# Optimization experiments

Measured on AMD Instinct MI355X. Metric: run time of the kernel, lower is better.

## Reference

```python
import jax, jax.numpy as jnp
import numpy as np

P, D, NF, NR, ND, EF, ER = 512, 128, 50000, 50000, 100000, 400000, 400000
BASELINE = 6.0


def setup_inputs() -> dict:
    key = jax.random.key(0)
    ctr = [0]
    def nk():
        ctr[0] += 1
        return jax.random.fold_in(key, ctr[0])
    def nrm(shape, scale=1.0):
        return jax.random.normal(nk(), shape, dtype=jnp.float32) * scale
    def uni(shape):
        return jax.random.uniform(nk(), shape, dtype=jnp.float32)
    def lin(fi, fo):
        return nrm((fi, fo), fi ** -0.5), jnp.zeros((fo,), jnp.float32)
    inp = {}
    inp['target_features'] = nrm((P,))
    inp['form_features'] = nrm((NF, P))
    inp['role_features'] = nrm((NR, P))
    inp['form_binds_y'] = BASELINE + nrm((EF,))
    inp['form_binds_w'] = uni((EF,))
    inp['role_binds_y'] = BASELINE + nrm((ER,))
    inp['role_binds_w'] = uni((ER,))
    inp['form_diff_w'] = uni((NF,)) + 0.01
    inp['role_diff_w'] = uni((NR,)) + 0.01
    inp['trust_vector'] = uni((3,))
    inp['drug_features'] = nrm((ND, D))
    inp['form_w1'], inp['form_b1'] = lin(P, P); inp['form_a1'] = jnp.full((1,), 0.25, jnp.float32)
    inp['form_w2'], inp['form_b2'] = lin(P, P)
    inp['role_w1'], inp['role_b1'] = lin(P, P); inp['role_a1'] = jnp.full((1,), 0.25, jnp.float32)
    inp['role_w2'], inp['role_b2'] = lin(P, P)
    inp['q_w'], inp['q_b'] = lin(P, D)
    inp['k_w'], inp['k_b'] = lin(D, D)
    inp['v_w'], inp['v_b'] = lin(D, D)
    inp['layer_emb'] = nrm((2, 16))
    inp['attn_w1'], inp['attn_b1'] = lin(2 * P + 16, 128)
    inp['attn_w2'], inp['attn_b2'] = lin(128, 64)
    inp['attn_w3'], inp['attn_b3'] = lin(64, 1)
    inp['mix_w1'], inp['mix_b1'] = lin(2 * D + 3, 64); inp['mix_a'] = jnp.full((1,), 0.25, jnp.float32)
    inp['mix_w2'], inp['mix_b2'] = lin(64, 2)
    inp['int_w1'], inp['int_b1'] = lin(D, P); inp['int_a'] = jnp.full((1,), 0.25, jnp.float32)
    inp['int_w2'], inp['int_b2'] = lin(P, P)
    inp['norm_w'] = jnp.ones((P,), jnp.float32)
    inp['norm_b'] = jnp.zeros((P,), jnp.float32)
    inp['delta_gate'] = jnp.float32(0.5)
    inp['form_neighbors'] = jnp.arange(NF, dtype=jnp.int32)
    inp['role_neighbors'] = jnp.arange(NR, dtype=jnp.int32)
    inp['form_binds_src'] = jax.random.randint(nk(), (EF,), 0, NF, dtype=jnp.int32)
    inp['form_binds_dst'] = jax.random.randint(nk(), (EF,), 0, ND, dtype=jnp.int32)
    inp['role_binds_src'] = jax.random.randint(nk(), (ER,), 0, NR, dtype=jnp.int32)
    inp['role_binds_dst'] = jax.random.randint(nk(), (ER,), 0, ND, dtype=jnp.int32)
    return inp


def _prelu(x, a):
    return jnp.where(x >= 0, x, a * x)


def _mlp2(x, w1, b1, a, w2, b2):
    return _prelu(x @ w1 + b1, a) @ w2 + b2


def _ln(x, w=None, b=None, eps=1e-5):
    m = jnp.mean(x, -1, keepdims=True)
    v = jnp.mean((x - m) ** 2, -1, keepdims=True)
    y = (x - m) * jax.lax.rsqrt(v + eps)
    return y if w is None else y * w + b


def _pref(z, nid, src, dst, y, w, drugs, q_w, q_b, k_w, k_b, v_w, v_b):
    # segment-softmax attention over (neighbor protein -> drug) bipartite edges
    N = nid.shape[0]
    order = jnp.argsort(nid)
    s = nid[order]
    pos = jnp.searchsorted(s, src)
    clip = jnp.minimum(pos, N - 1)
    valid = (pos < N) & (s[clip] == src)
    seg = jnp.where(valid, order[clip], N)  # invalid edges -> dump segment N
    q = z @ q_w + q_b                       # [D]
    d = drugs[dst]                          # [E, D] gather
    k = d @ k_w + k_b
    v = (d @ v_w + v_b) * ((y - BASELINE) * w)[:, None]
    logits = (k @ q) / (k.shape[-1] ** 0.5)
    mx = jax.ops.segment_max(logits, seg, num_segments=N + 1)
    mx = jnp.where(jnp.isfinite(mx), mx, 0.0)
    ex = jnp.where(valid, jnp.exp(logits - mx[seg]), 0.0)
    den = jax.ops.segment_sum(ex, seg, num_segments=N + 1) + 1e-12
    attn = ex / den[seg]
    return jax.ops.segment_sum(v * attn[:, None], seg, num_segments=N + 1)[:N]


def _attn_logits(z, zn, lemb, w1, b1, w2, b2, w3, b3):
    N = zn.shape[0]
    x = jnp.concatenate([jnp.broadcast_to(z, (N, z.shape[0])), zn,
                         jnp.broadcast_to(lemb, (N, lemb.shape[0]))], axis=-1)
    h = jax.nn.leaky_relu(x @ w1 + b1, 0.2)
    h = jax.nn.leaky_relu(h @ w2 + b2, 0.2)
    return (h @ w3 + b3)[:, 0]


def _core(fl, form_neighbors, role_neighbors, form_binds_src, form_binds_dst, role_binds_src, role_binds_dst):
    (target_features, form_features, role_features, form_binds_y, form_binds_w,
     role_binds_y, role_binds_w, form_diff_w, role_diff_w, trust_vector, drug_features,
     form_w1, form_b1, form_a1, form_w2, form_b2,
     role_w1, role_b1, role_a1, role_w2, role_b2,
     q_w, q_b, k_w, k_b, v_w, v_b, layer_emb,
     attn_w1, attn_b1, attn_w2, attn_b2, attn_w3, attn_b3,
     mix_w1, mix_b1, mix_a, mix_w2, mix_b2,
     int_w1, int_b1, int_a, int_w2, int_b2,
     norm_w, norm_b, delta_gate) = fl
    z_form = _mlp2(target_features, form_w1, form_b1, form_a1, form_w2, form_b2)
    z_role = _mlp2(target_features, role_w1, role_b1, role_a1, role_w2, role_b2)
    z = 0.5 * (z_form + z_role)
    form_feats = _mlp2(form_features, form_w1, form_b1, form_a1, form_w2, form_b2)
    role_feats = _mlp2(role_features, role_w1, role_b1, role_a1, role_w2, role_b2)
    form_msgs = _pref(z, form_neighbors, form_binds_src, form_binds_dst, form_binds_y, form_binds_w, drug_features, q_w, q_b, k_w, k_b, v_w, v_b)
    role_msgs = _pref(z, role_neighbors, role_binds_src, role_binds_dst, role_binds_y, role_binds_w, drug_features, q_w, q_b, k_w, k_b, v_w, v_b)
    form_logits = _attn_logits(z, form_feats, layer_emb[0], attn_w1, attn_b1, attn_w2, attn_b2, attn_w3, attn_b3)
    role_logits = _attn_logits(z, role_feats, layer_emb[1], attn_w1, attn_b1, attn_w2, attn_b2, attn_w3, attn_b3)
    form_attn = jax.nn.softmax(form_logits + jnp.log(jnp.maximum(form_diff_w, 1e-12)))
    role_attn = jax.nn.softmax(role_logits + jnp.log(jnp.maximum(role_diff_w, 1e-12)))
    v_form = form_attn @ form_msgs
    v_role = role_attn @ role_msgs
    mixer_in = jnp.concatenate([v_form, v_role, trust_vector])
    lw = jax.nn.softmax(_mlp2(mixer_in, mix_w1, mix_b1, mix_a, mix_w2, mix_b2))
    w_form, w_role = lw[0], lw[1]
    v_prior = w_form * v_form + w_role * v_role
    form_delta = form_attn @ (z[None, :] - form_feats)
    role_delta = role_attn @ (z[None, :] - role_feats)
    delta_raw = w_form * form_delta + w_role * role_delta
    delta_mean = delta_gate * _ln(delta_raw)
    z_refined = _ln(z + _mlp2(v_prior, int_w1, int_b1, int_a, int_w2, int_b2), norm_w, norm_b)
    return z_refined, v_prior, delta_mean


def reference(target_features, form_features, role_features, form_binds_y, form_binds_w, role_binds_y, role_binds_w, form_diff_w, role_diff_w, trust_vector, drug_features, form_w1, form_b1, form_a1, form_w2, form_b2, role_w1, role_b1, role_a1, role_w2, role_b2, q_w, q_b, k_w, k_b, v_w, v_b, layer_emb, attn_w1, attn_b1, attn_w2, attn_b2, attn_w3, attn_b3, mix_w1, mix_b1, mix_a, mix_w2, mix_b2, int_w1, int_b1, int_a, int_w2, int_b2, norm_w, norm_b, delta_gate, form_neighbors, role_neighbors, form_binds_src, form_binds_dst, role_binds_src, role_binds_dst):
    fl = (target_features, form_features, role_features, form_binds_y, form_binds_w,
          role_binds_y, role_binds_w, form_diff_w, role_diff_w, trust_vector, drug_features,
          form_w1, form_b1, form_a1, form_w2, form_b2,
          role_w1, role_b1, role_a1, role_w2, role_b2,
          q_w, q_b, k_w, k_b, v_w, v_b, layer_emb,
          attn_w1, attn_b1, attn_w2, attn_b2, attn_w3, attn_b3,
          mix_w1, mix_b1, mix_a, mix_w2, mix_b2,
          int_w1, int_b1, int_a, int_w2, int_b2,
          norm_w, norm_b, delta_gate)
    return _core(fl, form_neighbors, role_neighbors, form_binds_src, form_binds_dst, role_binds_src, role_binds_dst)
```

## Files before the change

kernel.cpp:

```cpp
#include <hip/hip_runtime.h>

#define NFN 50000
#define NDR 100000
#define NE  400000
#define MT  391
#define M0PAD 50048

__device__ __forceinline__ float bf2f(unsigned short u) {
    return __uint_as_float(((unsigned)u) << 16);
}
__device__ __forceinline__ unsigned short f2bf(float f) {
    unsigned u = __float_as_uint(f);
    unsigned r = 0x7FFFu + ((u >> 16) & 1u);
    return (unsigned short)((u + r) >> 16);
}

typedef __attribute__((ext_vector_type(8))) short bf16x8;
typedef __attribute__((ext_vector_type(4))) float f32x4;

struct KArgs {
    const float *tf, *ff, *rf, *fby, *fbw, *rby, *rbw, *fdw, *rdw, *trust, *drugs;
    const float *fw1, *fb1, *fa1, *fw2, *fb2, *rw1, *rb1, *ra1, *rw2, *rb2;
    const float *qw, *qb, *kw, *kb, *vw, *vb, *lemb;
    const float *aw1, *ab1, *aw2, *ab2, *aw3, *ab3;
    const float *mw1, *mb1, *ma, *mw2, *mb2;
    const float *iw1, *ib1, *ia, *iw2, *ib2;
    const float *nw, *nb, *dgate;
    const int *fsrc, *fdst, *rsrc, *rdst;
    float *shf, *shr;
    float *svf, *svr;
    float *gdenf, *gdenr;
    float *edenf, *edenr;
    float *cdf, *cdr;
    float *hraw;
    float *zraw;
    float *qraw;
    float *b1f, *b1r;
    float *sfr;
    float *o2raw;
    float *qk, *c0, *pe;
    unsigned short *w1tf, *w1tr;
    unsigned short *w2atf, *w2atr;
    unsigned short *aw2t;
    float *nexf, *nexr;
    unsigned short *H;
    unsigned short *Xb;
    float *hi;
    float *wfwr;
    float *out;
};

__global__ __launch_bounds__(512) void kA(KArgs A) {
    const int b = blockIdx.x;
    const int side = b >> 5, chunk = b & 31;
    const int tt = threadIdx.x;
    const float* w1 = side ? A.rw1 : A.fw1;
    float acc = 0.f;
    const int i0 = chunk * 16;
#pragma unroll
    for (int k = 0; k < 16; k++) {
        int i = i0 + k;
        acc = fmaf(A.tf[i], w1[(size_t)i * 512 + tt], acc);
    }
    atomicAdd(&A.hraw[side * 512 + tt], acc);
}

__global__ __launch_bounds__(512) void kB(KArgs A) {
    const int b = blockIdx.x;
    const int side = b >> 4, chunk = b & 15;
    const int tt = threadIdx.x;
    const float* w2 = side ? A.rw2 : A.fw2;
    const float* b1 = side ? A.rb1 : A.fb1;
    const float aa = (side ? A.ra1 : A.fa1)[0];
    float acc = 0.f;
    const int i0 = chunk * 32;
    for (int k = 0; k < 32; k++) {
        int i = i0 + k;
        float h = A.hraw[side * 512 + i] + b1[i];
        h = h >= 0.f ? h : aa * h;
        acc = fmaf(h, w2[(size_t)i * 512 + tt], acc);
    }
    if (b == 0) acc += A.fb2[tt] + A.rb2[tt];
    atomicAdd(&A.zraw[tt], acc);
}

__global__ __launch_bounds__(512) void kC1(KArgs A) {
    const int b = blockIdx.x;
    const int t = threadIdx.x;
    const int j = t & 127, isub = t >> 7;
    if (b < 8) {
        const int i0 = b * 64 + isub * 16;
        float acc = 0.f;
        for (int k = 0; k < 16; k++) {
            int i = i0 + k;
            acc = fmaf(0.5f * A.zraw[i], A.qw[(size_t)i * 128 + j], acc);
        }
        atomicAdd(&A.qraw[j], acc);
        if (b == 0 && t < 128) atomicAdd(&A.qraw[t], A.qb[t]);
    } else if (b < 16) {
        const int chunk = b - 8;
        const int i0 = chunk * 64 + isub * 16;
        float acc = 0.f;
        for (int k = 0; k < 16; k++) {
            int i = i0 + k;
            acc = fmaf(0.5f * A.zraw[i], A.aw1[(size_t)i * 128 + j], acc);
            acc = fmaf(A.fb2[i], A.aw1[(size_t)(512 + i) * 128 + j], acc);
        }
        atomicAdd(&A.b1f[j], acc);
        if (b == 8 && t < 128) {
            float c = A.ab1[t];
            for (int l = 0; l < 16; l++) c = fmaf(A.lemb[l], A.aw1[(size_t)(1024 + l) * 128 + t], c);
            atomicAdd(&A.b1f[t], c);
        }
    } else {
        const int chunk = b - 16;
        const int i0 = chunk * 64 + isub * 16;
        float acc = 0.f;
        for (int k = 0; k < 16; k++) {
            int i = i0 + k;
            acc = fmaf(0.5f * A.zraw[i], A.aw1[(size_t)i * 128 + j], acc);
            acc = fmaf(A.rb2[i], A.aw1[(size_t)(512 + i) * 128 + j], acc);
        }
        atomicAdd(&A.b1r[j], acc);
        if (b == 16 && t < 128) {
            float c = A.ab1[t];
            for (int l = 0; l < 16; l++) c = fmaf(A.lemb[16 + l], A.aw1[(size_t)(1024 + l) * 128 + t], c);
            atomicAdd(&A.b1r[t], c);
        }
    }
}

__global__ __launch_bounds__(256) void kC2(KArgs A) {
    const int t = threadIdx.x;
    __shared__ float sq[128];
    if (t < 128) sq[t] = A.qraw[t];
    __syncthreads();
    if (t < 128) {
        float s = 0.f;
        for (int j = 0; j < 128; j++) s = fmaf(A.kw[t * 128 + j], sq[j], s);
        A.qk[t] = s;
    } else if (t == 128) {
        float c = 0.f;
        for (int j = 0; j < 128; j++) c = fmaf(A.kb[j], sq[j], c);
        A.c0[0] = c;
    }
}

__global__ __launch_bounds__(256) void k_cvtX2(KArgs A) {
    const int XN4 = NFN * 512 / 4;
    const int P4 = M0PAD * 512 / 4;
    int idx = blockIdx.x * 256 + threadIdx.x;
    const int stride = gridDim.x * 256;
    for (; idx < 2 * XN4; idx += stride) {
        const int side = idx >= XN4;
        const int li = idx - side * XN4;
        float4 v = ((const float4*)(side ? A.rf : A.ff))[li];
        uint2 o;
        o.x = (unsigned)f2bf(v.x) | ((unsigned)f2bf(v.y) << 16);
        o.y = (unsigned)f2bf(v.z) | ((unsigned)f2bf(v.w) << 16);
        ((uint2*)A.Xb)[(size_t)side * P4 + li] = o;
    }
}

__global__ __launch_bounds__(512) void k_cvtW(KArgs A) {
    const int side = blockIdx.x >> 9;
    const int k = blockIdx.x & 511;
    const int n = threadIdx.x;
    const float* w1 = side ? A.rw1 : A.fw1;
    unsigned short* o = side ? A.w1tr : A.w1tf;
    o[(size_t)n * 512 + k] = f2bf(w1[k * 512 + n]);
}

__global__ __launch_bounds__(128) void k_cvtA2(KArgs A) {
    const int j = blockIdx.x;
    const int i = threadIdx.x;
    A.aw2t[j * 128 + i] = f2bf(A.aw2[i * 64 + j]);
}

__global__ __launch_bounds__(128) void k_w2a(KArgs A) {
    const int side = blockIdx.x >> 9;
    const int i = blockIdx.x & 511;
    const int j = threadIdx.x;
    const float* w2 = side ? A.rw2 : A.fw2;
    unsigned short* outp = side ? A.w2atr : A.w2atf;
    float s = 0.f;
    for (int k = 0; k < 512; k++)
        s = fmaf(w2[i * 512 + k], A.aw1[(size_t)(512 + k) * 128 + j], s);
    outp[(size_t)j * 512 + i] = f2bf(s);
}

__global__ __launch_bounds__(256, 2)
void mfma_gemm(KArgs A) {
    __shared__ __align__(16) unsigned short Abuf[2][128 * 32];
    __shared__ __align__(16) unsigned short Bbuf[2][128 * 32];
    const int t = threadIdx.x;
    const int lane = t & 63, wv = t >> 6;
    const int p = blockIdx.x;
    const int L = (p & 7) * MT + (p >> 3);
    const int side = L >= (MT * 4);
    const int lbid = L - side * (MT * 4);
    const int m0l = (lbid >> 2) * 128, n0 = (lbid & 3) * 128;
    const unsigned short* __restrict__ Ab = A.Xb + (size_t)side * M0PAD * 512;
    const unsigned short* __restrict__ Bt = side ? A.w1tr : A.w1tf;
    const float* __restrict__ bias = side ? A.rb1 : A.fb1;
    const float aval = (side ? A.ra1 : A.fa1)[0];
    unsigned short* __restrict__ Cv = A.H + (size_t)side * M0PAD * 512;
    const int wm = (wv >> 1) * 64, wn = (wv & 1) * 64;
    const int lm = lane & 15, ko = lane >> 4;
    const int K = 512;

    f32x4 acc[4][4];
#pragma unroll
    for (int i = 0; i < 4; i++)
#pragma unroll
        for (int j = 0; j < 4; j++) acc[i][j] = (f32x4){0.f, 0.f, 0.f, 0.f};

    auto stage = [&](int buf, int k0) {
#pragma unroll
        for (int ii = 0; ii < 2; ii++) {
            const int inst = wv * 2 + ii;
            const int rl = inst * 16 + (lane >> 2);
            const int sl = (lane & 3) ^ ((rl >> 1) & 3);
            int ar = m0l + rl; if (ar >= NFN) ar = NFN - 1;
            __builtin_amdgcn_global_load_lds(
                (const __attribute__((address_space(1))) void*)(Ab + (size_t)ar * K + k0 + sl * 8),
                (__attribute__((address_space(3))) void*)(&Abuf[buf][inst * 512]), 16, 0, 0);
            __builtin_amdgcn_global_load_lds(
                (const __attribute__((address_space(1))) void*)(Bt + (size_t)(n0 + rl) * K + k0 + sl * 8),
                (__attribute__((address_space(3))) void*)(&Bbuf[buf][inst * 512]), 16, 0, 0);
        }
    };

    auto compute = [&](int buf) {
        bf16x8 af[4], bfr[4];
#pragma unroll
        for (int mi = 0; mi < 4; mi++) {
            int row = wm + mi * 16 + lm;
            af[mi] = *(const bf16x8*)&Abuf[buf][row * 32 + ((ko ^ ((row >> 1) & 3)) * 8)];
        }
#pragma unroll
        for (int ni = 0; ni < 4; ni++) {
            int col = wn + ni * 16 + lm;
            bfr[ni] = *(const bf16x8*)&Bbuf[buf][col * 32 + ((ko ^ ((col >> 1) & 3)) * 8)];
        }
#pragma unroll
        for (int mi = 0; mi < 4; mi++)
#pragma unroll
            for (int ni = 0; ni < 4; ni++)
                acc[mi][ni] = __builtin_amdgcn_mfma_f32_16x16x32_bf16(af[mi], bfr[ni], acc[mi][ni], 0, 0, 0);
    };

    stage(0, 0);
    __syncthreads();
    for (int kt = 0; kt < 16; kt++) {
        if (kt + 1 < 16) stage((kt + 1) & 1, (kt + 1) * 32);
        compute(kt & 1);
        __syncthreads();
    }

#pragma unroll
    for (int mi = 0; mi < 4; mi++) {
#pragma unroll
        for (int reg = 0; reg < 4; reg++) {
            int row = m0l + wm + mi * 16 + ko * 4 + reg;
#pragma unroll
            for (int ni = 0; ni < 4; ni++) {
                int col = n0 + wn + ni * 16 + lm;
                float v = acc[mi][ni][reg] + bias[col];
                v = v >= 0.f ? v : aval * v;
                Cv[(size_t)row * 512 + col] = f2bf(v);
            }
        }
    }
}

__global__ __launch_bounds__(256, 2)
void gemm_logits(KArgs A) {
    __shared__ __align__(16) unsigned short Abuf[2][128 * 32];
    __shared__ __align__(16) unsigned short Bbuf[2][128 * 32];
    __shared__ __align__(16) unsigned short Gs[128][136];
    __shared__ float ps[128];
    __shared__ float red2[128];
    __shared__ float snex[128];
    const int bid = blockIdx.x;
    const int side = bid >= MT;
    const int m0l = (bid - side * MT) * 128;
    const unsigned short* __restrict__ Ab = A.H + (size_t)side * M0PAD * 512;
    const unsigned short* __restrict__ Bt = side ? A.w2atr : A.w2atf;
    const float* __restrict__ bias = side ? A.b1r : A.b1f;
    const float* __restrict__ dw = side ? A.rdw : A.fdw;
    float* __restrict__ nex = side ? A.nexr : A.nexf;
    float* __restrict__ gden = side ? A.gdenr : A.gdenf;
    const int t = threadIdx.x;
    const int lane = t & 63, wv = t >> 6;
    const int wm = (wv >> 1) * 64, wn = (wv & 1) * 64;
    const int lm = lane & 15, ko = lane >> 4;
    const int K = 512;

    f32x4 acc[4][4];
#pragma unroll
    for (int i = 0; i < 4; i++)
#pragma unroll
        for (int j = 0; j < 4; j++) acc[i][j] = (f32x4){0.f, 0.f, 0.f, 0.f};

    auto stage = [&](int buf, int k0) {
#pragma unroll
        for (int ii = 0; ii < 2; ii++) {
            const int inst = wv * 2 + ii;
            const int rl = inst * 16 + (lane >> 2);
            const int sl = (lane & 3) ^ ((rl >> 1) & 3);
            int ar = m0l + rl; if (ar >= NFN) ar = NFN - 1;
            __builtin_amdgcn_global_load_lds(
                (const __attribute__((address_space(1))) void*)(Ab + (size_t)ar * K + k0 + sl * 8),
                (__attribute__((address_space(3))) void*)(&Abuf[buf][inst * 512]), 16, 0, 0);
            __builtin_amdgcn_global_load_lds(
                (const __attribute__((address_space(1))) void*)(Bt + (size_t)rl * K + k0 + sl * 8),
                (__attribute__((address_space(3))) void*)(&Bbuf[buf][inst * 512]), 16, 0, 0);
        }
    };

    auto compute = [&](int buf) {
        bf16x8 af[4], bfr[4];
#pragma unroll
        for (int mi = 0; mi < 4; mi++) {
            int row = wm + mi * 16 + lm;
            af[mi] = *(const bf16x8*)&Abuf[buf][row * 32 + ((ko ^ ((row >> 1) & 3)) * 8)];
        }
#pragma unroll
        for (int ni = 0; ni < 4; ni++) {
            int col = wn + ni * 16 + lm;
            bfr[ni] = *(const bf16x8*)&Bbuf[buf][col * 32 + ((ko ^ ((col >> 1) & 3)) * 8)];
        }
#pragma unroll
        for (int mi = 0; mi < 4; mi++)
#pragma unroll
            for (int ni = 0; ni < 4; ni++)
                acc[mi][ni] = __builtin_amdgcn_mfma_f32_16x16x32_bf16(af[mi], bfr[ni], acc[mi][ni], 0, 0, 0);
    };

    stage(0, 0);
    __syncthreads();
    for (int kt = 0; kt < 16; kt++) {
        if (kt + 1 < 16) stage((kt + 1) & 1, (kt + 1) * 32);
        compute(kt & 1);
        __syncthreads();
    }

#pragma unroll
    for (int mi = 0; mi < 4; mi++) {
#pragma unroll
        for (int reg = 0; reg < 4; reg++) {
            int row_l = wm + mi * 16 + ko * 4 + reg;
#pragma unroll
            for (int ni = 0; ni < 4; ni++) {
                int col = wn + ni * 16 + lm;
                float v = acc[mi][ni][reg] + bias[col];
                v = v >= 0.f ? v : 0.2f * v;
                Gs[row_l][col] = f2bf(v);
            }
        }
    }
    __syncthreads();

    const int wr0 = wv * 32;
    float ab2v[4], aw3v[4];
#pragma unroll
    for (int ni = 0; ni < 4; ni++) {
        int col = ni * 16 + lm;
        ab2v[ni] = A.ab2[col];
        aw3v[ni] = A.aw3[col];
    }
    f32x4 acc2[2][4];
#pragma unroll
    for (int i = 0; i < 2; i++)
#pragma unroll
        for (int j = 0; j < 4; j++) acc2[i][j] = (f32x4){0.f, 0.f, 0.f, 0.f};
#pragma unroll
    for (int kk = 0; kk < 4; kk++) {
        bf16x8 ga[2], bb[4];
#pragma unroll
        for (int mi = 0; mi < 2; mi++)
            ga[mi] = *(const bf16x8*)&Gs[wr0 + mi * 16 + lm][kk * 32 + ko * 8];
#pragma unroll
        for (int ni = 0; ni < 4; ni++)
            bb[ni] = *(const bf16x8*)(A.aw2t + (size_t)(ni * 16 + lm) * 128 + kk * 32 + ko * 8);
#pragma unroll
        for (int mi = 0; mi < 2; mi++)
#pragma unroll
            for (int ni = 0; ni < 4; ni++)
                acc2[mi][ni] = __builtin_amdgcn_mfma_f32_16x16x32_bf16(ga[mi], bb[ni], acc2[mi][ni], 0, 0, 0);
    }
#pragma unroll
    for (int mi = 0; mi < 2; mi++) {
#pragma unroll
        for (int reg = 0; reg < 4; reg++) {
            float s = 0.f;
#pragma unroll
            for (int ni = 0; ni < 4; ni++) {
                float v = acc2[mi][ni][reg] + ab2v[ni];
                v = v >= 0.f ? v : 0.2f * v;
                s = fmaf(v, aw3v[ni], s);
            }
            s += __shfl_xor(s, 1, 64);
            s += __shfl_xor(s, 2, 64);
            s += __shfl_xor(s, 4, 64);
            s += __shfl_xor(s, 8, 64);
            if (lm == 0) ps[wr0 + mi * 16 + ko * 4 + reg] = s;
        }
    }
    __syncthreads();
    float val = 0.f;
    if (t < 128) {
        int node = m0l + t;
        if (node < NFN) {
            val = expf(ps[t] + A.ab3[0] + logf(fmaxf(dw[node], 1e-12f)));
            nex[node] = val;
        }
        snex[t] = val;
        red2[t] = val;
    }
    __syncthreads();
    if (t < 64) red2[t] += red2[t + 64];
    __syncthreads();
    if (t < 32) red2[t] += red2[t + 32];
    __syncthreads();
    if (t < 16) red2[t] += red2[t + 16];
    __syncthreads();
    if (t == 0) {
        float s = 0.f;
        for (int i = 0; i < 16; i++) s += red2[i];
        atomicAdd(gden, s);
    }
    {
        const unsigned short* Hrow = Ab + (size_t)m0l * 512;
        float a0 = 0.f, a1 = 0.f;
        for (int r = 0; r < 128; r += 2) {
            const float w0 = snex[r], w1 = snex[r + 1];
            const unsigned v0 = *(const unsigned*)(Hrow + (size_t)r * 512 + 2 * t);
            const unsigned v1 = *(const unsigned*)(Hrow + (size_t)(r + 1) * 512 + 2 * t);
            a0 = fmaf(w0, bf2f((unsigned short)(v0 & 0xFFFFu)), a0);
            a1 = fmaf(w0, bf2f((unsigned short)(v0 >> 16)), a1);
            a0 = fmaf(w1, bf2f((unsigned short)(v1 & 0xFFFFu)), a0);
            a1 = fmaf(w1, bf2f((unsigned short)(v1 >> 16)), a1);
        }
        float* SH = side ? A.shr : A.shf;
        atomicAdd(&SH[2 * t], a0);
        atomicAdd(&SH[2 * t + 1], a1);
    }
}

__global__ __launch_bounds__(256) void k_pd(KArgs A) {
    const int lane = threadIdx.x & 63;
    const int gw = blockIdx.x * 4 + (threadIdx.x >> 6);
    const int nw = gridDim.x * 4;
    const float2 qk2 = *(const float2*)(A.qk + 2 * lane);
    const float c0 = A.c0[0];
    for (int dr = gw; dr < NDR; dr += nw) {
        float2 dv = *(const float2*)(A.drugs + (size_t)dr * 128 + 2 * lane);
        float p = fmaf(dv.x, qk2.x, dv.y * qk2.y);
        for (int off = 32; off >= 1; off >>= 1) p += __shfl_xor(p, off, 64);
        if (lane == 0) A.pe[dr] = expf((p + c0) * 0.088388347648318447f);
    }
}

__global__ __launch_bounds__(256) void k_edge1(KArgs A) {
    const int side = blockIdx.y;
    const int* src = side ? A.rsrc : A.fsrc;
    const int* dst = side ? A.rdst : A.fdst;
    float* eden = side ? A.edenr : A.edenf;
    const int base = blockIdx.x * 1024 + threadIdx.x;
#pragma unroll
    for (int u = 0; u < 4; u++) {
        const int e = base + u * 256;
        if (e < NE) atomicAdd(&eden[src[e]], A.pe[dst[e]]);
    }
}

__global__ __launch_bounds__(256) void k_nfac(KArgs A) {
    const int side = blockIdx.y;
    const int n = blockIdx.x * 256 + threadIdx.x;
    if (n >= NFN) return;
    const float* nex = side ? A.nexr : A.nexf;
    float* eden = side ? A.edenr : A.edenf;
    const float invden = 1.0f / *(side ? A.gdenr : A.gdenf);
    eden[n] = nex[n] * invden / (eden[n] + 1e-12f);
}

__global__ __launch_bounds__(256) void k_edge2(KArgs A) {
    const int side = blockIdx.y;
    const int* src = side ? A.rsrc : A.fsrc;
    const int* dst = side ? A.rdst : A.fdst;
    const float* yy = side ? A.rby : A.fby;
    const float* ww = side ? A.rbw : A.fbw;
    const float* fac = side ? A.edenr : A.edenf;
    float* cd = side ? A.cdr : A.cdf;
    float* sv = side ? A.svr : A.svf;
    const int base = blockIdx.x * 1024 + threadIdx.x;
    float csum = 0.f;
#pragma unroll
    for (int u = 0; u < 4; u++) {
        const int e = base + u * 256;
        if (e < NE) {
            float coef = fac[src[e]] * A.pe[dst[e]] * ((yy[e] - 6.0f) * ww[e]);
            atomicAdd(&cd[dst[e]], coef);
            csum += coef;
        }
    }
    __shared__ float red[256];
    red[threadIdx.x] = csum; __syncthreads();
    for (int s2 = 128; s2 >= 1; s2 >>= 1) {
        if (threadIdx.x < s2) red[threadIdx.x] += red[threadIdx.x + s2];
        __syncthreads();
    }
    if (threadIdx.x == 0) atomicAdd(&sv[128], red[0]);
}

__global__ __launch_bounds__(256) void k_wsumD(KArgs A) {
    const int t = threadIdx.x;
    const int col = t & 127, rg = t >> 7;
    __shared__ float red[2][2][128];
    float af = 0.f, ar = 0.f;
    for (int dr = blockIdx.x * 2 + rg; dr < NDR; dr += gridDim.x * 2) {
        float cf = A.cdf[dr], cr = A.cdr[dr];
        float dv = A.drugs[(size_t)dr * 128 + col];
        af = fmaf(cf, dv, af);
        ar = fmaf(cr, dv, ar);
    }
    red[rg][0][col] = af; red[rg][1][col] = ar;
    __syncthreads();
    if (rg == 0) {
        atomicAdd(&A.svf[col], red[0][0][col] + red[1][0][col]);
        atomicAdd(&A.svr[col], red[0][1][col] + red[1][1][col]);
    }
}

__global__ __launch_bounds__(512) void kF1(KArgs A) {
    const int b = blockIdx.x;
    const int side = b >> 3, chunk = b & 7;
    const int tt = threadIdx.x;
    const float* w2 = side ? A.rw2 : A.fw2;
    const float* SH = side ? A.shr : A.shf;
    const float invden = 1.0f / *(side ? A.gdenr : A.gdenf);
    float acc = 0.f;
    const int i0 = chunk * 64;
    for (int k = 0; k < 64; k++) {
        int i = i0 + k;
        acc = fmaf(SH[i], w2[(size_t)i * 512 + tt], acc);
    }
    acc *= invden;
    if (chunk == 0) acc += (side ? A.rb2 : A.fb2)[tt];
    atomicAdd(&A.sfr[side * 512 + tt], acc);
}

__global__ __launch_bounds__(512) void kF2(KArgs A) {
    const int t = threadIdx.x;
    __shared__ float vform[128], vrole[128], vprior[128], mh[64], sw[2];
    if (t < 128) {
        float vf = A.svf[128] * A.vb[t];
        float vr = A.svr[128] * A.vb[t];
        for (int i = 0; i < 128; i++) {
            vf = fmaf(A.svf[i], A.vw[i * 128 + t], vf);
            vr = fmaf(A.svr[i], A.vw[i * 128 + t], vr);
        }
        vform[t] = vf; vrole[t] = vr;
    }
    __syncthreads();
    if (t < 64) {
        float m = A.mb1[t];
        for (int i = 0; i < 128; i++) m = fmaf(vform[i], A.mw1[i * 64 + t], m);
        for (int i = 0; i < 128; i++) m = fmaf(vrole[i], A.mw1[(128 + i) * 64 + t], m);
        for (int i = 0; i < 3; i++)   m = fmaf(A.trust[i], A.mw1[(256 + i) * 64 + t], m);
        float ma = A.ma[0];
        mh[t] = m >= 0.f ? m : ma * m;
    }
    __syncthreads();
    if (t < 2) {
        float o = A.mb2[t];
        for (int i = 0; i < 64; i++) o = fmaf(mh[i], A.mw2[i * 2 + t], o);
        sw[t] = o;
    }
    __syncthreads();
    const float mo = fmaxf(sw[0], sw[1]);
    const float e0 = expf(sw[0] - mo), e1 = expf(sw[1] - mo);
    const float wf = e0 / (e0 + e1), wr = e1 / (e0 + e1);
    if (t == 0) { A.wfwr[0] = wf; A.wfwr[1] = wr; }
    if (t < 128) {
        float vp = wf * vform[t] + wr * vrole[t];
        vprior[t] = vp;
        A.out[512 + t] = vp;
    }
    __syncthreads();
    float hi = A.ib1[t];
    for (int i = 0; i < 128; i++) hi = fmaf(vprior[i], A.iw1[(size_t)i * 512 + t], hi);
    float ia = A.ia[0];
    A.hi[t] = hi >= 0.f ? hi : ia * hi;
}

__global__ __launch_bounds__(512) void kF3(KArgs A) {
    const int chunk = blockIdx.x;
    const int tt = threadIdx.x;
    float acc = 0.f;
    const int i0 = chunk * 64;
    for (int k = 0; k < 64; k++) {
        int i = i0 + k;
        acc = fmaf(A.hi[i], A.iw2[(size_t)i * 512 + tt], acc);
    }
    if (chunk == 0) acc += A.ib2[tt];
    atomicAdd(&A.o2raw[tt], acc);
}

__global__ __launch_bounds__(512) void kF4(KArgs A) {
    const int t = threadIdx.x;
    __shared__ float red[512];
    const float wf = A.wfwr[0], wr = A.wfwr[1];
    const float zv = 0.5f * A.zraw[t];
    float dr_ = zv - wf * A.sfr[t] - wr * A.sfr[512 + t];
    red[t] = dr_; __syncthreads();
    for (int s = 256; s >= 1; s >>= 1) { if (t < s) red[t] += red[t + s]; __syncthreads(); }
    float mean = red[0] * (1.f / 512.f); __syncthreads();
    float dd = dr_ - mean;
    red[t] = dd * dd; __syncthreads();
    for (int s = 256; s >= 1; s >>= 1) { if (t < s) red[t] += red[t + s]; __syncthreads(); }
    float var = red[0] * (1.f / 512.f); __syncthreads();
    A.out[640 + t] = A.dgate[0] * (dd * rsqrtf(var + 1e-5f));
    float zin = zv + A.o2raw[t];
    red[t] = zin; __syncthreads();
    for (int s = 256; s >= 1; s >>= 1) { if (t < s) red[t] += red[t + s]; __syncthreads(); }
    float mean2 = red[0] * (1.f / 512.f); __syncthreads();
    float d2 = zin - mean2;
    red[t] = d2 * d2; __syncthreads();
    for (int s = 256; s >= 1; s >>= 1) { if (t < s) red[t] += red[t + s]; __syncthreads(); }
    float var2 = red[0] * (1.f / 512.f);
    A.out[t] = (d2 * rsqrtf(var2 + 1e-5f)) * A.nw[t] + A.nb[t];
}

extern "C" void kernel_launch(void* const* d_in, const int* in_sizes, int n_in,
                              void* d_out, int out_size, void* d_ws, size_t ws_size,
                              hipStream_t stream) {
    (void)in_sizes; (void)n_in; (void)out_size;
    KArgs A;
    A.tf    = (const float*)d_in[0];
    A.ff    = (const float*)d_in[1];
    A.rf    = (const float*)d_in[2];
    A.fby   = (const float*)d_in[3];
    A.fbw   = (const float*)d_in[4];
    A.rby   = (const float*)d_in[5];
    A.rbw   = (const float*)d_in[6];
    A.fdw   = (const float*)d_in[7];
    A.rdw   = (const float*)d_in[8];
    A.trust = (const float*)d_in[9];
    A.drugs = (const float*)d_in[10];
    A.fw1 = (const float*)d_in[11]; A.fb1 = (const float*)d_in[12]; A.fa1 = (const float*)d_in[13];
    A.fw2 = (const float*)d_in[14]; A.fb2 = (const float*)d_in[15];
    A.rw1 = (const float*)d_in[16]; A.rb1 = (const float*)d_in[17]; A.ra1 = (const float*)d_in[18];
    A.rw2 = (const float*)d_in[19]; A.rb2 = (const float*)d_in[20];
    A.qw = (const float*)d_in[21]; A.qb = (const float*)d_in[22];
    A.kw = (const float*)d_in[23]; A.kb = (const float*)d_in[24];
    A.vw = (const float*)d_in[25]; A.vb = (const float*)d_in[26];
    A.lemb = (const float*)d_in[27];
    A.aw1 = (const float*)d_in[28]; A.ab1 = (const float*)d_in[29];
    A.aw2 = (const float*)d_in[30]; A.ab2 = (const float*)d_in[31];
    A.aw3 = (const float*)d_in[32]; A.ab3 = (const float*)d_in[33];
    A.mw1 = (const float*)d_in[34]; A.mb1 = (const float*)d_in[35]; A.ma = (const float*)d_in[36];
    A.mw2 = (const float*)d_in[37]; A.mb2 = (const float*)d_in[38];
    A.iw1 = (const float*)d_in[39]; A.ib1 = (const float*)d_in[40]; A.ia = (const float*)d_in[41];
    A.iw2 = (const float*)d_in[42]; A.ib2 = (const float*)d_in[43];
    A.nw = (const float*)d_in[44]; A.nb = (const float*)d_in[45];
    A.dgate = (const float*)d_in[46];
    A.fsrc = (const int*)d_in[49];
    A.fdst = (const int*)d_in[50];
    A.rsrc = (const int*)d_in[51];
    A.rdst = (const int*)d_in[52];
    A.out = (float*)d_out;

    char* w = (char*)d_ws;
    size_t off = 0;
    auto alloc = [&](size_t bytes) -> void* {
        void* p = w + off;
        off = (off + bytes + 255) & ~(size_t)255;
        return p;
    };
    A.shf   = (float*)alloc(512 * 4);
    A.shr   = (float*)alloc(512 * 4);
    A.svf   = (float*)alloc(129 * 4);
    A.svr   = (float*)alloc(129 * 4);
    A.gdenf = (float*)alloc(4);
    A.gdenr = (float*)alloc(4);
    A.edenf = (float*)alloc((size_t)NFN * 4);
    A.edenr = (float*)alloc((size_t)NFN * 4);
    A.cdf   = (float*)alloc((size_t)NDR * 4);
    A.cdr   = (float*)alloc((size_t)NDR * 4);
    A.hraw  = (float*)alloc(1024 * 4);
    A.zraw  = (float*)alloc(512 * 4);
    A.qraw  = (float*)alloc(128 * 4);
    A.b1f   = (float*)alloc(128 * 4);
    A.b1r   = (float*)alloc(128 * 4);
    A.sfr   = (float*)alloc(1024 * 4);
    A.o2raw = (float*)alloc(512 * 4);
    const size_t zbytes = off;
    A.qk   = (float*)alloc(128 * 4);
    A.c0   = (float*)alloc(4);
    A.pe   = (float*)alloc((size_t)NDR * 4);
    A.w1tf = (unsigned short*)alloc((size_t)512 * 512 * 2);
    A.w1tr = (unsigned short*)alloc((size_t)512 * 512 * 2);
    A.w2atf = (unsigned short*)alloc((size_t)128 * 512 * 2);
    A.w2atr = (unsigned short*)alloc((size_t)128 * 512 * 2);
    A.aw2t  = (unsigned short*)alloc((size_t)64 * 128 * 2);
    A.nexf  = (float*)alloc((size_t)NFN * 4);
    A.nexr  = (float*)alloc((size_t)NFN * 4);
    A.H     = (unsigned short*)alloc((size_t)2 * M0PAD * 512 * 2);
    A.Xb    = (unsigned short*)alloc((size_t)2 * M0PAD * 512 * 2);
    A.hi    = (float*)alloc(512 * 4);
    A.wfwr  = (float*)alloc(2 * 4);
    if (ws_size && off > ws_size) return;

    hipMemsetAsync(d_ws, 0, zbytes, stream);

    kA<<<64, 512, 0, stream>>>(A);
    kB<<<32, 512, 0, stream>>>(A);
    kC1<<<24, 512, 0, stream>>>(A);
    kC2<<<1, 256, 0, stream>>>(A);
    k_cvtW<<<1024, 512, 0, stream>>>(A);
    k_cvtA2<<<64, 128, 0, stream>>>(A);
    k_w2a<<<1024, 128, 0, stream>>>(A);
    k_pd<<<1024, 256, 0, stream>>>(A);

    const int EB4 = (NE + 1023) / 1024;
    const int NFB = (NFN + 255) / 256;
    k_cvtX2<<<2048, 256, 0, stream>>>(A);
    mfma_gemm<<<2 * MT * 4, 256, 0, stream>>>(A);
    gemm_logits<<<2 * MT, 256, 0, stream>>>(A);
    k_edge1<<<dim3(EB4, 2), 256, 0, stream>>>(A);
    k_nfac<<<dim3(NFB, 2), 256, 0, stream>>>(A);
    k_edge2<<<dim3(EB4, 2), 256, 0, stream>>>(A);
    k_wsumD<<<512, 256, 0, stream>>>(A);
    kF1<<<16, 512, 0, stream>>>(A);
    kF2<<<1, 512, 0, stream>>>(A);
    kF3<<<8, 512, 0, stream>>>(A);
    kF4<<<1, 512, 0, stream>>>(A);
}
```

Measured before the change: 486.1 us.

## Fuse fp32-to-bf16 feature conversion into GEMM staging and merge small kernels

Drops the separate pass that converted the form/role feature matrices to bf16. The GEMM now streams fp32 rows straight into LDS through a new XOR swizzle and packs them to bf16 in registers before the MFMA, which removes a full write and re-read of a large intermediate buffer. Conversion now truncates instead of rounding to nearest, and the fp32 A tile doubles that tile's LDS use and its global read traffic. Separately, the weight-prep kernels are merged into one launch, and kF1 and kF2 share one launch. The kF1/kF2 merge risks a race if kF2 reads the sfr values that kF1 accumulates.

```diff
diff --git a/kernel.cpp b/kernel.cpp
--- a/kernel.cpp
+++ b/kernel.cpp
@@ -13,6 +13,9 @@
     unsigned u = __float_as_uint(f);
     unsigned r = 0x7FFFu + ((u >> 16) & 1u);
     return (unsigned short)((u + r) >> 16);
+}
+__device__ __forceinline__ unsigned bpack(float lo, float hi) {
+    return (__float_as_uint(hi) & 0xFFFF0000u) | (__float_as_uint(lo) >> 16);
 }
 
 typedef __attribute__((ext_vector_type(8))) short bf16x8;
@@ -44,7 +47,6 @@
     unsigned short *aw2t;
     float *nexf, *nexr;
     unsigned short *H;
-    unsigned short *Xb;
     float *hi;
     float *wfwr;
     float *out;
@@ -146,52 +148,36 @@
     }
 }
 
-__global__ __launch_bounds__(256) void k_cvtX2(KArgs A) {
-    const int XN4 = NFN * 512 / 4;
-    const int P4 = M0PAD * 512 / 4;
-    int idx = blockIdx.x * 256 + threadIdx.x;
-    const int stride = gridDim.x * 256;
-    for (; idx < 2 * XN4; idx += stride) {
-        const int side = idx >= XN4;
-        const int li = idx - side * XN4;
-        float4 v = ((const float4*)(side ? A.rf : A.ff))[li];
-        uint2 o;
-        o.x = (unsigned)f2bf(v.x) | ((unsigned)f2bf(v.y) << 16);
-        o.y = (unsigned)f2bf(v.z) | ((unsigned)f2bf(v.w) << 16);
-        ((uint2*)A.Xb)[(size_t)side * P4 + li] = o;
-    }
-}
-
-__global__ __launch_bounds__(512) void k_cvtW(KArgs A) {
-    const int side = blockIdx.x >> 9;
-    const int k = blockIdx.x & 511;
-    const int n = threadIdx.x;
-    const float* w1 = side ? A.rw1 : A.fw1;
-    unsigned short* o = side ? A.w1tr : A.w1tf;
-    o[(size_t)n * 512 + k] = f2bf(w1[k * 512 + n]);
-}
-
-__global__ __launch_bounds__(128) void k_cvtA2(KArgs A) {
-    const int j = blockIdx.x;
-    const int i = threadIdx.x;
-    A.aw2t[j * 128 + i] = f2bf(A.aw2[i * 64 + j]);
-}
-
-__global__ __launch_bounds__(128) void k_w2a(KArgs A) {
-    const int side = blockIdx.x >> 9;
-    const int i = blockIdx.x & 511;
-    const int j = threadIdx.x;
-    const float* w2 = side ? A.rw2 : A.fw2;
-    unsigned short* outp = side ? A.w2atr : A.w2atf;
-    float s = 0.f;
-    for (int k = 0; k < 512; k++)
-        s = fmaf(w2[i * 512 + k], A.aw1[(size_t)(512 + k) * 128 + j], s);
-    outp[(size_t)j * 512 + i] = f2bf(s);
+__global__ __launch_bounds__(512) void k_prep(KArgs A) {
+    const int b = blockIdx.x;
+    const int t = threadIdx.x;
+    if (b < 1024) {
+        const int side = b >> 9;
+        const int k = b & 511;
+        const float* w1 = side ? A.rw1 : A.fw1;
+        unsigned short* o = side ? A.w1tr : A.w1tf;
+        o[(size_t)t * 512 + k] = f2bf(w1[k * 512 + t]);
+    } else if (b < 1280) {
+        const int lb = b - 1024;
+        const int side = lb >> 7;
+        const int i = (lb & 127) * 4 + (t >> 7);
+        const int j = t & 127;
+        const float* w2 = side ? A.rw2 : A.fw2;
+        unsigned short* outp = side ? A.w2atr : A.w2atf;
+        float s = 0.f;
+        for (int k = 0; k < 512; k++)
+            s = fmaf(w2[i * 512 + k], A.aw1[(size_t)(512 + k) * 128 + j], s);
+        outp[(size_t)j * 512 + i] = f2bf(s);
+    } else {
+        const int elem = (b - 1280) * 512 + t;
+        const int j = elem >> 7, i = elem & 127;
+        A.aw2t[j * 128 + i] = f2bf(A.aw2[i * 64 + j]);
+    }
 }
 
 __global__ __launch_bounds__(256, 2)
 void mfma_gemm(KArgs A) {
-    __shared__ __align__(16) unsigned short Abuf[2][128 * 32];
+    __shared__ __align__(16) float Afb[2][128 * 32];
     __shared__ __align__(16) unsigned short Bbuf[2][128 * 32];
     const int t = threadIdx.x;
     const int lane = t & 63, wv = t >> 6;
@@ -200,7 +186,7 @@
     const int side = L >= (MT * 4);
     const int lbid = L - side * (MT * 4);
     const int m0l = (lbid >> 2) * 128, n0 = (lbid & 3) * 128;
-    const unsigned short* __restrict__ Ab = A.Xb + (size_t)side * M0PAD * 512;
+    const float* __restrict__ Xf = side ? A.rf : A.ff;
     const unsigned short* __restrict__ Bt = side ? A.w1tr : A.w1tf;
     const float* __restrict__ bias = side ? A.rb1 : A.fb1;
     const float aval = (side ? A.ra1 : A.fa1)[0];
@@ -217,14 +203,20 @@
 
     auto stage = [&](int buf, int k0) {
 #pragma unroll
+        for (int ii = 0; ii < 4; ii++) {
+            const int inst = wv * 4 + ii;
+            const int rl = inst * 8 + (lane >> 3);
+            const int sl = (lane & 7) ^ (rl & 7);
+            int ar = m0l + rl; if (ar >= NFN) ar = NFN - 1;
+            __builtin_amdgcn_global_load_lds(
+                (const __attribute__((address_space(1))) void*)(Xf + (size_t)ar * K + k0 + sl * 4),
+                (__attribute__((address_space(3))) void*)(&Afb[buf][inst * 256]), 16, 0, 0);
+        }
+#pragma unroll
         for (int ii = 0; ii < 2; ii++) {
             const int inst = wv * 2 + ii;
             const int rl = inst * 16 + (lane >> 2);
             const int sl = (lane & 3) ^ ((rl >> 1) & 3);
-            int ar = m0l + rl; if (ar >= NFN) ar = NFN - 1;
-            __builtin_amdgcn_global_load_lds(
-                (const __attribute__((address_space(1))) void*)(Ab + (size_t)ar * K + k0 + sl * 8),
-                (__attribute__((address_space(3))) void*)(&Abuf[buf][inst * 512]), 16, 0, 0);
             __builtin_amdgcn_global_load_lds(
                 (const __attribute__((address_space(1))) void*)(Bt + (size_t)(n0 + rl) * K + k0 + sl * 8),
                 (__attribute__((address_space(3))) void*)(&Bbuf[buf][inst * 512]), 16, 0, 0);
@@ -236,7 +228,16 @@
 #pragma unroll
         for (int mi = 0; mi < 4; mi++) {
             int row = wm + mi * 16 + lm;
-            af[mi] = *(const bf16x8*)&Abuf[buf][row * 32 + ((ko ^ ((row >> 1) & 3)) * 8)];
+            int s0 = (ko * 2) ^ (row & 7);
+            int s1 = (ko * 2 + 1) ^ (row & 7);
+            f32x4 fa = *(const f32x4*)&Afb[buf][row * 32 + s0 * 4];
+            f32x4 fb = *(const f32x4*)&Afb[buf][row * 32 + s1 * 4];
+            unsigned u0 = bpack(fa[0], fa[1]);
+            unsigned u1 = bpack(fa[2], fa[3]);
+            unsigned u2 = bpack(fb[0], fb[1]);
+            unsigned u3 = bpack(fb[2], fb[3]);
+            uint4 uu = make_uint4(u0, u1, u2, u3);
+            af[mi] = *(bf16x8*)&uu;
         }
 #pragma unroll
         for (int ni = 0; ni < 4; ni++) {
@@ -534,26 +535,25 @@
     }
 }
 
-__global__ __launch_bounds__(512) void kF1(KArgs A) {
+__global__ __launch_bounds__(512) void kF12(KArgs A) {
     const int b = blockIdx.x;
-    const int side = b >> 3, chunk = b & 7;
-    const int tt = threadIdx.x;
-    const float* w2 = side ? A.rw2 : A.fw2;
-    const float* SH = side ? A.shr : A.shf;
-    const float invden = 1.0f / *(side ? A.gdenr : A.gdenf);
-    float acc = 0.f;
-    const int i0 = chunk * 64;
-    for (int k = 0; k < 64; k++) {
-        int i = i0 + k;
-        acc = fmaf(SH[i], w2[(size_t)i * 512 + tt], acc);
-    }
-    acc *= invden;
-    if (chunk == 0) acc += (side ? A.rb2 : A.fb2)[tt];
-    atomicAdd(&A.sfr[side * 512 + tt], acc);
-}
-
-__global__ __launch_bounds__(512) void kF2(KArgs A) {
     const int t = threadIdx.x;
+    if (b < 16) {
+        const int side = b >> 3, chunk = b & 7;
+        const float* w2 = side ? A.rw2 : A.fw2;
+        const float* SH = side ? A.shr : A.shf;
+        const float invden = 1.0f / *(side ? A.gdenr : A.gdenf);
+        float acc = 0.f;
+        const int i0 = chunk * 64;
+        for (int k = 0; k < 64; k++) {
+            int i = i0 + k;
+            acc = fmaf(SH[i], w2[(size_t)i * 512 + t], acc);
+        }
+        acc *= invden;
+        if (chunk == 0) acc += (side ? A.rb2 : A.fb2)[t];
+        atomicAdd(&A.sfr[side * 512 + t], acc);
+        return;
+    }
     __shared__ float vform[128], vrole[128], vprior[128], mh[64], sw[2];
     if (t < 128) {
         float vf = A.svf[128] * A.vb[t];
@@ -709,7 +709,6 @@
     A.nexf  = (float*)alloc((size_t)NFN * 4);
     A.nexr  = (float*)alloc((size_t)NFN * 4);
     A.H     = (unsigned short*)alloc((size_t)2 * M0PAD * 512 * 2);
-    A.Xb    = (unsigned short*)alloc((size_t)2 * M0PAD * 512 * 2);
     A.hi    = (float*)alloc(512 * 4);
     A.wfwr  = (float*)alloc(2 * 4);
     if (ws_size && off > ws_size) return;
@@ -720,22 +719,18 @@
     kB<<<32, 512, 0, stream>>>(A);
     kC1<<<24, 512, 0, stream>>>(A);
     kC2<<<1, 256, 0, stream>>>(A);
-    k_cvtW<<<1024, 512, 0, stream>>>(A);
-    k_cvtA2<<<64, 128, 0, stream>>>(A);
-    k_w2a<<<1024, 128, 0, stream>>>(A);
+    k_prep<<<1296, 512, 0, stream>>>(A);
     k_pd<<<1024, 256, 0, stream>>>(A);
 
     const int EB4 = (NE + 1023) / 1024;
     const int NFB = (NFN + 255) / 256;
-    k_cvtX2<<<2048, 256, 0, stream>>>(A);
     mfma_gemm<<<2 * MT * 4, 256, 0, stream>>>(A);
     gemm_logits<<<2 * MT, 256, 0, stream>>>(A);
     k_edge1<<<dim3(EB4, 2), 256, 0, stream>>>(A);
     k_nfac<<<dim3(NFB, 2), 256, 0, stream>>>(A);
     k_edge2<<<dim3(EB4, 2), 256, 0, stream>>>(A);
     k_wsumD<<<512, 256, 0, stream>>>(A);
-    kF1<<<16, 512, 0, stream>>>(A);
-    kF2<<<1, 512, 0, stream>>>(A);
+    kF12<<<17, 512, 0, stream>>>(A);
     kF3<<<8, 512, 0, stream>>>(A);
     kF4<<<1, 512, 0, stream>>>(A);
 }
```

Result: faster. 472.4 us (-2.8%).
